# Kernel tuning notes

Hardware: AMD Instinct MI355X
Metric: run time of the kernel (lower is better)

Reference implementation:

```python
import jax, jax.numpy as jnp
import numpy as np

DIM_MODEL = 1024
NUM_HEADS = 16
DIM_HEAD = 64
B, S = 2, 2048


def setup_inputs() -> dict:
    key = jax.random.key(0)
    ks = jax.random.split(key, 10)
    scale = 1.0 / np.sqrt(DIM_MODEL)
    inp = {
        "x": jax.random.normal(ks[0], (B, S, DIM_MODEL), dtype=jnp.float32),
        "padding_mask": jax.random.randint(ks[1], (B, S), 0, 2, dtype=jnp.int32),
        "Wq": jax.random.normal(ks[2], (DIM_MODEL, DIM_MODEL), dtype=jnp.float32) * scale,
        "bq": jnp.zeros((DIM_MODEL,), dtype=jnp.float32),
        "Wk": jax.random.normal(ks[3], (DIM_MODEL, DIM_MODEL), dtype=jnp.float32) * scale,
        "bk": jnp.zeros((DIM_MODEL,), dtype=jnp.float32),
        "Wv": jax.random.normal(ks[4], (DIM_MODEL, DIM_MODEL), dtype=jnp.float32) * scale,
        "bv": jnp.zeros((DIM_MODEL,), dtype=jnp.float32),
        "Wo": jax.random.normal(ks[5], (DIM_MODEL, DIM_MODEL), dtype=jnp.float32) * scale,
        "bo": jnp.zeros((DIM_MODEL,), dtype=jnp.float32),
    }
    return inp


def reference(x, padding_mask, Wq, bq, Wk, bk, Wv, bv, Wo, bo):
    b, s, _ = x.shape
    dot_scale = jnp.sqrt(jnp.asarray(DIM_HEAD, dtype=x.dtype))
    # projections -> (b, h, s, d)
    q = (x @ Wq + bq).reshape(b, s, NUM_HEADS, DIM_HEAD).transpose(0, 2, 1, 3)
    k = (x @ Wk + bk).reshape(b, s, NUM_HEADS, DIM_HEAD).transpose(0, 2, 1, 3)
    v = (x @ Wv + bv).reshape(b, s, NUM_HEADS, DIM_HEAD).transpose(0, 2, 1, 3)
    # scores (b, h, s, s)
    scores = jnp.einsum("bhqd,bhkd->bhqk", q, k) / dot_scale
    mask = (padding_mask == 1)[:, None, None, :]  # (b,1,1,s) over key positions
    scores = jnp.where(mask, -jnp.inf, scores)
    attn = jax.nn.softmax(scores, axis=-1)
    out = jnp.einsum("bhqk,bhkd->bhqd", attn, v)
    out = out.transpose(0, 2, 1, 3).reshape(b, s, NUM_HEADS * DIM_HEAD)
    return out @ Wo + bo
```

## Files before the change

### kernel.cpp

```cpp
#include <hip/hip_runtime.h>
#include <hip/hip_bf16.h>
#include <stdint.h>
#include <math.h>

#define D_MODEL 1024
#define NHEAD   16
#define DHEAD   64
#define BATCH   2
#define SEQ     2048
#define M_TOK   (BATCH * SEQ)

#define QSCALE 0.18033688011112042f

typedef __attribute__((ext_vector_type(8))) short   short8;
typedef __attribute__((ext_vector_type(8))) __bf16  bf16x8;
typedef __attribute__((ext_vector_type(4))) float   f32x4;

__device__ inline short f2bf(float f) {
  unsigned int u = __builtin_bit_cast(unsigned int, f);
  unsigned int r = (u + 0x7FFFu + ((u >> 16) & 1u)) >> 16;
  return (short)(unsigned short)r;
}
__device__ inline short f2bf_fast(float f) {
  unsigned int u = __builtin_bit_cast(unsigned int, f);
  return (short)(unsigned short)((u + 0x8000u) >> 16);
}

__device__ inline void gl_lds16(const void* g, void* l) {
  __builtin_amdgcn_global_load_lds((__attribute__((address_space(1))) void*)(g),
                                   (__attribute__((address_space(3))) void*)(l),
                                   16, 0, 0);
}

__device__ inline bf16x8 lds_frag(const short* p) {
  return *(const bf16x8*)(p);
}
__device__ inline bf16x8 lds_frag64(const short* p) {
  union { bf16x8 v; short4 h[2]; } u;
  u.h[0] = *(const short4*)(p);
  u.h[1] = *(const short4*)(p + 4);
  return u.v;
}

__global__ __launch_bounds__(256) void prep(const float* __restrict__ x,
                                            short* __restrict__ xb,
                                            const float* __restrict__ w0,
                                            const float* __restrict__ w1,
                                            const float* __restrict__ w2,
                                            const float* __restrict__ w3,
                                            short* __restrict__ out) {
  const int t = threadIdx.x;
  if (blockIdx.z == 4) {
    size_t base = ((size_t)blockIdx.y * 16 + blockIdx.x) * 16384;
    const float* in = x + base;
    short* o = xb + base;
#pragma unroll
    for (int i = 0; i < 16; ++i) {
      f32x4 v = *(const f32x4*)(in + (size_t)t * 4 + i * 1024);
      short4 s4;
      s4.x = f2bf(v[0]); s4.y = f2bf(v[1]); s4.z = f2bf(v[2]); s4.w = f2bf(v[3]);
      *(short4*)(o + (size_t)t * 4 + i * 1024) = s4;
    }
    return;
  }
  __shared__ short tile[64][72];
  const float* W = blockIdx.z == 0 ? w0 : blockIdx.z == 1 ? w1 : blockIdx.z == 2 ? w2 : w3;
  short* O = out + (size_t)blockIdx.z * (D_MODEL * (size_t)D_MODEL);
  int n0 = blockIdx.x * 64, k0 = blockIdx.y * 64;
#pragma unroll
  for (int i = 0; i < 16; ++i) {
    int idx = t + 256 * i;
    int r = idx >> 6, c = idx & 63;
    tile[r][c] = f2bf(W[(size_t)(k0 + r) * D_MODEL + n0 + c]);
  }
  __syncthreads();
#pragma unroll
  for (int i = 0; i < 16; ++i) {
    int idx = t + 256 * i;
    int r = idx >> 6, c = idx & 63;
    O[(size_t)(n0 + r) * D_MODEL + k0 + c] = tile[c][r];
  }
}

template <bool OUTF32, bool VT, int TN>
__global__ __launch_bounds__(256) void gemm128(const short* __restrict__ A,
                                               const short* __restrict__ Bt_base,
                                               const float* __restrict__ b0,
                                               const float* __restrict__ b1,
                                               const float* __restrict__ b2,
                                               void* __restrict__ out_base,
                                               short* __restrict__ vt,
                                               const int* __restrict__ pm) {
  constexpr int NI = TN / 32;
  const int z = blockIdx.z;
  const short* Bt   = Bt_base + (size_t)z * (D_MODEL * (size_t)D_MODEL);
  const float* bias = (z == 0) ? b0 : (z == 1) ? b1 : b2;

  __shared__ short As[128 * 64];
  __shared__ short Bs[TN * 64];

  const int t = threadIdx.x;
  const int lane = t & 63;
  const int wid = t >> 6;
  const int wm = (wid >> 1) * 64, wn = (wid & 1) * (TN / 2);
  const int m0 = blockIdx.x * 128, n0 = blockIdx.y * TN;
  const int cl = lane & 15, q = lane >> 4;
  const int sw = cl & 7;

  f32x4 acc[4][NI];
#pragma unroll
  for (int i = 0; i < 4; ++i)
#pragma unroll
    for (int j = 0; j < NI; ++j) acc[i][j] = 0.0f;

  for (int k0 = 0; k0 < D_MODEL; k0 += 64) {
    __syncthreads();
#pragma unroll
    for (int i = 0; i < 4; ++i) {
      int c = t + 256 * i;
      int row = c >> 3, cp = c & 7;
      int col = ((cp ^ (row & 7)) * 8);
      gl_lds16(A + (size_t)(m0 + row) * D_MODEL + k0 + col, (void*)(As + c * 8));
    }
#pragma unroll
    for (int i = 0; i < NI; ++i) {
      int c = t + 256 * i;
      int row = c >> 3, cp = c & 7;
      int col = ((cp ^ (row & 7)) * 8);
      gl_lds16(Bt + (size_t)(n0 + row) * D_MODEL + k0 + col, (void*)(Bs + c * 8));
    }
    __syncthreads();

    bf16x8 af[4][2], bfr[NI][2];
#pragma unroll
    for (int mi = 0; mi < 4; ++mi) {
      af[mi][0] = lds_frag(As + (wm + mi * 16 + cl) * 64 + (q ^ sw) * 8);
      af[mi][1] = lds_frag(As + (wm + mi * 16 + cl) * 64 + ((4 + q) ^ sw) * 8);
    }
#pragma unroll
    for (int ni = 0; ni < NI; ++ni) {
      bfr[ni][0] = lds_frag(Bs + (wn + ni * 16 + cl) * 64 + (q ^ sw) * 8);
      bfr[ni][1] = lds_frag(Bs + (wn + ni * 16 + cl) * 64 + ((4 + q) ^ sw) * 8);
    }
#pragma unroll
    for (int mi = 0; mi < 4; ++mi)
#pragma unroll
      for (int ni = 0; ni < NI; ++ni) {
        acc[mi][ni] = __builtin_amdgcn_mfma_f32_16x16x32_bf16(af[mi][0], bfr[ni][0], acc[mi][ni], 0, 0, 0);
        acc[mi][ni] = __builtin_amdgcn_mfma_f32_16x16x32_bf16(af[mi][1], bfr[ni][1], acc[mi][ni], 0, 0, 0);
      }
  }

  const float oscale = (VT && z == 0) ? QSCALE : 1.0f;
  int4 mm[4];
  if (VT && z == 2) {
#pragma unroll
    for (int mi = 0; mi < 4; ++mi) {
      int rbase = m0 + wm + mi * 16 + q * 4;
      mm[mi] = *(const int4*)(pm + (size_t)(rbase >> 11) * SEQ + (rbase & (SEQ - 1)));
    }
  }
#pragma unroll
  for (int ni = 0; ni < NI; ++ni) {
    int col = n0 + wn + ni * 16 + cl;
    float bv = bias[col];
#pragma unroll
    for (int mi = 0; mi < 4; ++mi) {
      int rbase = m0 + wm + mi * 16 + q * 4;
      if (VT && z == 2) {
        short4 o4;
        o4.x = (mm[mi].x == 1) ? (short)0 : f2bf_fast(acc[mi][ni][0] + bv);
        o4.y = (mm[mi].y == 1) ? (short)0 : f2bf_fast(acc[mi][ni][1] + bv);
        o4.z = (mm[mi].z == 1) ? (short)0 : f2bf_fast(acc[mi][ni][2] + bv);
        o4.w = (mm[mi].w == 1) ? (short)0 : f2bf_fast(acc[mi][ni][3] + bv);
        int btok = rbase >> 11;
        int s    = rbase & (SEQ - 1);
        *(short4*)(vt + (size_t)btok * ((size_t)D_MODEL * SEQ) + (size_t)col * SEQ + s) = o4;
      } else {
#pragma unroll
        for (int r = 0; r < 4; ++r) {
          float v = (acc[mi][ni][r] + bv) * oscale;
          size_t idx = (size_t)(rbase + r) * D_MODEL + col;
          if (OUTF32) {
            ((float*)out_base)[idx] = v;
          } else {
            short* out = (short*)out_base + (size_t)z * ((size_t)M_TOK * D_MODEL);
            out[idx] = f2bf_fast(v);
          }
        }
      }
    }
  }
}

__global__ __launch_bounds__(256) void attn_flash(const short* __restrict__ Q,
                                                  const short* __restrict__ K,
                                                  const short* __restrict__ Vt,
                                                  const int*   __restrict__ mask,
                                                  short* __restrict__ ctx) {
  const int qb = blockIdx.x;
  const int h  = blockIdx.y;
  const int b  = blockIdx.z;

  __shared__ short QPs[8704];
  __shared__ short Ks[64 * 64];
  __shared__ short Vts[64 * 64];
  __shared__ short Us[64];

  const int t = threadIdx.x;
  const int lane = t & 63;
  const int wid = t >> 6;
  const int cl = lane & 15, q = lane >> 4;
  const int sw = cl & 7;

  const size_t rowQ0 = (size_t)b * SEQ + (size_t)qb * 128;
  const size_t rowK0 = (size_t)b * SEQ;
  const size_t vbase = ((size_t)b * D_MODEL + h * DHEAD) * SEQ;

#pragma unroll
  for (int i = 0; i < 4; ++i) {
    int c = t + 256 * i;
    int row = c >> 3, cp = c & 7;
    gl_lds16(Q + (rowQ0 + row) * D_MODEL + h * DHEAD + ((cp ^ (row & 7)) * 8),
             (void*)(QPs + c * 8));
  }
  __syncthreads();

  bf16x8 qf[2][2];
#pragma unroll
  for (int rb = 0; rb < 2; ++rb) {
    int row = wid * 32 + rb * 16 + cl;
    qf[rb][0] = lds_frag(QPs + row * 64 + (q ^ sw) * 8);
    qf[rb][1] = lds_frag(QPs + row * 64 + ((4 + q) ^ sw) * 8);
  }
  short* Psw = QPs + wid * (32 * 68);

  f32x4 lacc[2], oacc[2][4];
#pragma unroll
  for (int rb = 0; rb < 2; ++rb) {
    lacc[rb] = 0.0f;
#pragma unroll
    for (int dj = 0; dj < 4; ++dj) oacc[rb][dj] = 0.0f;
  }

  for (int kv0 = 0; kv0 < SEQ; kv0 += 64) {
    __syncthreads();

#pragma unroll
    for (int i = 0; i < 2; ++i) {
      int c = t + 256 * i;
      int row = c >> 3, cp = c & 7;
      gl_lds16(K + (rowK0 + kv0 + row) * D_MODEL + h * DHEAD + ((cp ^ (row & 7)) * 8),
               (void*)(Ks + c * 8));
      gl_lds16(Vt + vbase + (size_t)row * SEQ + kv0 + ((cp ^ (row & 7)) * 8),
               (void*)(Vts + c * 8));
    }
    if (t < 64) Us[t] = (mask[(size_t)b * SEQ + kv0 + t] == 1) ? (short)0 : (short)0x3F80;
    __syncthreads();

    f32x4 s[2][4];
#pragma unroll
    for (int j = 0; j < 4; ++j) {
      bf16x8 kf0 = lds_frag(Ks + (j * 16 + cl) * 64 + (q ^ sw) * 8);
      bf16x8 kf1 = lds_frag(Ks + (j * 16 + cl) * 64 + ((4 + q) ^ sw) * 8);
#pragma unroll
      for (int rb = 0; rb < 2; ++rb) {
        f32x4 sa = 0.0f;
        sa = __builtin_amdgcn_mfma_f32_16x16x32_bf16(qf[rb][0], kf0, sa, 0, 0, 0);
        sa = __builtin_amdgcn_mfma_f32_16x16x32_bf16(qf[rb][1], kf1, sa, 0, 0, 0);
        s[rb][j] = sa;
      }
    }

#pragma unroll
    for (int rb = 0; rb < 2; ++rb)
#pragma unroll
      for (int j = 0; j < 4; ++j)
#pragma unroll
        for (int r = 0; r < 4; ++r)
          Psw[(rb * 16 + q * 4 + r) * 68 + j * 16 + cl] = f2bf_fast(exp2f(s[rb][j][r]));

    asm volatile("" ::: "memory");

    bf16x8 pf[2][2];
#pragma unroll
    for (int rb = 0; rb < 2; ++rb) {
      pf[rb][0] = lds_frag64(Psw + (rb * 16 + cl) * 68 + q * 8);
      pf[rb][1] = lds_frag64(Psw + (rb * 16 + cl) * 68 + 32 + q * 8);
    }
    bf16x8 uf0 = lds_frag(Us + q * 8);
    bf16x8 uf1 = lds_frag(Us + 32 + q * 8);
#pragma unroll
    for (int dj = 0; dj < 4; ++dj) {
      bf16x8 vf0 = lds_frag(Vts + (dj * 16 + cl) * 64 + (q ^ sw) * 8);
      bf16x8 vf1 = lds_frag(Vts + (dj * 16 + cl) * 64 + ((4 + q) ^ sw) * 8);
#pragma unroll
      for (int rb = 0; rb < 2; ++rb) {
        oacc[rb][dj] = __builtin_amdgcn_mfma_f32_16x16x32_bf16(pf[rb][0], vf0, oacc[rb][dj], 0, 0, 0);
        oacc[rb][dj] = __builtin_amdgcn_mfma_f32_16x16x32_bf16(pf[rb][1], vf1, oacc[rb][dj], 0, 0, 0);
      }
    }
#pragma unroll
    for (int rb = 0; rb < 2; ++rb) {
      lacc[rb] = __builtin_amdgcn_mfma_f32_16x16x32_bf16(pf[rb][0], uf0, lacc[rb], 0, 0, 0);
      lacc[rb] = __builtin_amdgcn_mfma_f32_16x16x32_bf16(pf[rb][1], uf1, lacc[rb], 0, 0, 0);
    }
  }

#pragma unroll
  for (int rb = 0; rb < 2; ++rb)
#pragma unroll
    for (int dj = 0; dj < 4; ++dj)
#pragma unroll
      for (int r = 0; r < 4; ++r) {
        float lv = lacc[rb][r];
        float o = (lv > 0.0f) ? oacc[rb][dj][r] / lv : 0.0f;
        size_t row = rowQ0 + wid * 32 + rb * 16 + q * 4 + r;
        ctx[row * D_MODEL + h * DHEAD + dj * 16 + cl] = f2bf(o);
      }
}

extern "C" void kernel_launch(void* const* d_in, const int* in_sizes, int n_in,
                              void* d_out, int out_size, void* d_ws, size_t ws_size,
                              hipStream_t stream) {
  (void)in_sizes; (void)n_in; (void)out_size; (void)ws_size;

  const float* x  = (const float*)d_in[0];
  const int*   pm = (const int*)  d_in[1];
  const float* Wq = (const float*)d_in[2];
  const float* bq = (const float*)d_in[3];
  const float* Wk = (const float*)d_in[4];
  const float* bk = (const float*)d_in[5];
  const float* Wv = (const float*)d_in[6];
  const float* bv = (const float*)d_in[7];
  const float* Wo = (const float*)d_in[8];
  const float* bo = (const float*)d_in[9];

  const size_t WMAT = (size_t)D_MODEL * D_MODEL;
  const size_t TOKD = (size_t)M_TOK * D_MODEL;

  short* base = (short*)d_ws;
  short* Wt = base;
  short* xb = base + 4 * WMAT;
  short* Qw = xb + TOKD;
  short* Kw = Qw + TOKD;
  short* Vtw = Kw + TOKD;
  short* Cw = Vtw + TOKD;

  prep<<<dim3(16, 16, 5), 256, 0, stream>>>(x, xb, Wq, Wk, Wv, Wo, Wt);
  gemm128<false, true, 128><<<dim3(M_TOK / 128, D_MODEL / 128, 3), 256, 0, stream>>>(
      xb, Wt, bq, bk, bv, Qw, Vtw, pm);
  attn_flash<<<dim3(SEQ / 128, NHEAD, BATCH), 256, 0, stream>>>(Qw, Kw, Vtw, pm, Cw);
  gemm128<true, false, 64><<<dim3(M_TOK / 128, D_MODEL / 64, 1), 256, 0, stream>>>(
      Cw, Wt + 3 * WMAT, bo, bo, bo, d_out, nullptr, nullptr);
}
```

Baseline: 223.6 us.

## Split attention KV range across two wave groups with LDS reduction

```diff
diff --git a/kernel.cpp b/kernel.cpp
--- a/kernel.cpp
+++ b/kernel.cpp
@@ -193,7 +193,7 @@
   }
 }
 
-__global__ __launch_bounds__(256) void attn_flash(const short* __restrict__ Q,
+__global__ __launch_bounds__(512) void attn_flash(const short* __restrict__ Q,
                                                   const short* __restrict__ K,
                                                   const short* __restrict__ Vt,
                                                   const int*   __restrict__ mask,
@@ -202,14 +202,16 @@
   const int h  = blockIdx.y;
   const int b  = blockIdx.z;
 
-  __shared__ short QPs[8704];
-  __shared__ short Ks[64 * 64];
-  __shared__ short Vts[64 * 64];
-  __shared__ short Us[64];
+  __shared__ __align__(16) short QPs[17408];
+  __shared__ __align__(16) short Ks[2 * 64 * 64];
+  __shared__ __align__(16) short Vts[2 * 64 * 64];
+  __shared__ __align__(16) short Us[2 * 64];
 
   const int t = threadIdx.x;
   const int lane = t & 63;
   const int wid = t >> 6;
+  const int wg  = wid >> 1;
+  const int kvh = wid & 1;
   const int cl = lane & 15, q = lane >> 4;
   const int sw = cl & 7;
 
@@ -218,8 +220,8 @@
   const size_t vbase = ((size_t)b * D_MODEL + h * DHEAD) * SEQ;
 
 #pragma unroll
-  for (int i = 0; i < 4; ++i) {
-    int c = t + 256 * i;
+  for (int i = 0; i < 2; ++i) {
+    int c = t + 512 * i;
     int row = c >> 3, cp = c & 7;
     gl_lds16(Q + (rowQ0 + row) * D_MODEL + h * DHEAD + ((cp ^ (row & 7)) * 8),
              (void*)(QPs + c * 8));
@@ -229,11 +231,14 @@
   bf16x8 qf[2][2];
 #pragma unroll
   for (int rb = 0; rb < 2; ++rb) {
-    int row = wid * 32 + rb * 16 + cl;
+    int row = wg * 32 + rb * 16 + cl;
     qf[rb][0] = lds_frag(QPs + row * 64 + (q ^ sw) * 8);
     qf[rb][1] = lds_frag(QPs + row * 64 + ((4 + q) ^ sw) * 8);
   }
   short* Psw = QPs + wid * (32 * 68);
+  const short* Kp = Ks  + kvh * 4096;
+  const short* Vp = Vts + kvh * 4096;
+  const short* Up = Us  + kvh * 64;
 
   f32x4 lacc[2], oacc[2][4];
 #pragma unroll
@@ -243,26 +248,31 @@
     for (int dj = 0; dj < 4; ++dj) oacc[rb][dj] = 0.0f;
   }
 
-  for (int kv0 = 0; kv0 < SEQ; kv0 += 64) {
+  for (int s0 = 0; s0 < 1024; s0 += 64) {
     __syncthreads();
 
-#pragma unroll
-    for (int i = 0; i < 2; ++i) {
-      int c = t + 256 * i;
-      int row = c >> 3, cp = c & 7;
-      gl_lds16(K + (rowK0 + kv0 + row) * D_MODEL + h * DHEAD + ((cp ^ (row & 7)) * 8),
-               (void*)(Ks + c * 8));
-      gl_lds16(Vt + vbase + (size_t)row * SEQ + kv0 + ((cp ^ (row & 7)) * 8),
-               (void*)(Vts + c * 8));
-    }
-    if (t < 64) Us[t] = (mask[(size_t)b * SEQ + kv0 + t] == 1) ? (short)0 : (short)0x3F80;
+    {
+      int row = t >> 3, cp = t & 7;
+      int col = (cp ^ (row & 7)) * 8;
+      gl_lds16(K + (rowK0 + s0 + row) * D_MODEL + h * DHEAD + col,
+               (void*)(Ks + t * 8));
+      gl_lds16(K + (rowK0 + 1024 + s0 + row) * D_MODEL + h * DHEAD + col,
+               (void*)(Ks + 4096 + t * 8));
+      gl_lds16(Vt + vbase + (size_t)row * SEQ + s0 + col,
+               (void*)(Vts + t * 8));
+      gl_lds16(Vt + vbase + (size_t)row * SEQ + 1024 + s0 + col,
+               (void*)(Vts + 4096 + t * 8));
+    }
+    if (t < 128)
+      Us[t] = (mask[(size_t)b * SEQ + (t >> 6) * 1024 + s0 + (t & 63)] == 1)
+                  ? (short)0 : (short)0x3F80;
     __syncthreads();
 
     f32x4 s[2][4];
 #pragma unroll
     for (int j = 0; j < 4; ++j) {
-      bf16x8 kf0 = lds_frag(Ks + (j * 16 + cl) * 64 + (q ^ sw) * 8);
-      bf16x8 kf1 = lds_frag(Ks + (j * 16 + cl) * 64 + ((4 + q) ^ sw) * 8);
+      bf16x8 kf0 = lds_frag(Kp + (j * 16 + cl) * 64 + (q ^ sw) * 8);
+      bf16x8 kf1 = lds_frag(Kp + (j * 16 + cl) * 64 + ((4 + q) ^ sw) * 8);
 #pragma unroll
       for (int rb = 0; rb < 2; ++rb) {
         f32x4 sa = 0.0f;
@@ -288,12 +298,12 @@
       pf[rb][0] = lds_frag64(Psw + (rb * 16 + cl) * 68 + q * 8);
       pf[rb][1] = lds_frag64(Psw + (rb * 16 + cl) * 68 + 32 + q * 8);
     }
-    bf16x8 uf0 = lds_frag(Us + q * 8);
-    bf16x8 uf1 = lds_frag(Us + 32 + q * 8);
+    bf16x8 uf0 = lds_frag(Up + q * 8);
+    bf16x8 uf1 = lds_frag(Up + 32 + q * 8);
 #pragma unroll
     for (int dj = 0; dj < 4; ++dj) {
-      bf16x8 vf0 = lds_frag(Vts + (dj * 16 + cl) * 64 + (q ^ sw) * 8);
-      bf16x8 vf1 = lds_frag(Vts + (dj * 16 + cl) * 64 + ((4 + q) ^ sw) * 8);
+      bf16x8 vf0 = lds_frag(Vp + (dj * 16 + cl) * 64 + (q ^ sw) * 8);
+      bf16x8 vf1 = lds_frag(Vp + (dj * 16 + cl) * 64 + ((4 + q) ^ sw) * 8);
 #pragma unroll
       for (int rb = 0; rb < 2; ++rb) {
         oacc[rb][dj] = __builtin_amdgcn_mfma_f32_16x16x32_bf16(pf[rb][0], vf0, oacc[rb][dj], 0, 0, 0);
@@ -307,6 +317,34 @@
     }
   }
 
+  __syncthreads();
+  float* redO = (float*)QPs;
+  float* redL = (float*)Ks;
+  const int rbase = (wg * 64 + lane) * 32;
+  const int lbase = (wg * 64 + lane) * 8;
+  if (kvh) {
+#pragma unroll
+    for (int rb = 0; rb < 2; ++rb) {
+#pragma unroll
+      for (int dj = 0; dj < 4; ++dj) {
+        int qi = (rb * 4 + dj) ^ (lane & 7);
+        *(f32x4*)(redO + rbase + qi * 4) = oacc[rb][dj];
+      }
+      *(f32x4*)(redL + lbase + rb * 4) = lacc[rb];
+    }
+  }
+  __syncthreads();
+  if (kvh) return;
+#pragma unroll
+  for (int rb = 0; rb < 2; ++rb) {
+    lacc[rb] += *(const f32x4*)(redL + lbase + rb * 4);
+#pragma unroll
+    for (int dj = 0; dj < 4; ++dj) {
+      int qi = (rb * 4 + dj) ^ (lane & 7);
+      oacc[rb][dj] += *(const f32x4*)(redO + rbase + qi * 4);
+    }
+  }
+
 #pragma unroll
   for (int rb = 0; rb < 2; ++rb)
 #pragma unroll
@@ -315,7 +353,7 @@
       for (int r = 0; r < 4; ++r) {
         float lv = lacc[rb][r];
         float o = (lv > 0.0f) ? oacc[rb][dj][r] / lv : 0.0f;
-        size_t row = rowQ0 + wid * 32 + rb * 16 + q * 4 + r;
+        size_t row = rowQ0 + wg * 32 + rb * 16 + q * 4 + r;
         ctx[row * D_MODEL + h * DHEAD + dj * 16 + cl] = f2bf(o);
       }
 }
@@ -350,7 +388,7 @@
   prep<<<dim3(16, 16, 5), 256, 0, stream>>>(x, xb, Wq, Wk, Wv, Wo, Wt);
   gemm128<false, true, 128><<<dim3(M_TOK / 128, D_MODEL / 128, 3), 256, 0, stream>>>(
       xb, Wt, bq, bk, bv, Qw, Vtw, pm);
-  attn_flash<<<dim3(SEQ / 128, NHEAD, BATCH), 256, 0, stream>>>(Qw, Kw, Vtw, pm, Cw);
+  attn_flash<<<dim3(SEQ / 128, NHEAD, BATCH), 512, 0, stream>>>(Qw, Kw, Vtw, pm, Cw);
   gemm128<true, false, 64><<<dim3(M_TOK / 128, D_MODEL / 64, 1), 256, 0, stream>>>(
       Cw, Wt + 3 * WMAT, bo, bo, bo, d_out, nullptr, nullptr);
 }
```

New measurement: 214.4 us. 1.04x faster.
